# Kernel tuning notes

Measured on AMD Instinct MI355X. Metric: run time of the kernel, lower is better.

## Reference

```python
import jax, jax.numpy as jnp
import numpy as np

IGNORE_INDEX = 0


def _lovasz_softmax(inputs, targets):
    # inputs: [B, C, H, W] logits; targets: [B, H, W] int class ids
    C = inputs.shape[1]
    probs = jax.nn.softmax(inputs, axis=1)                      # [B,C,H,W]
    probs_flat = probs.transpose(0, 2, 3, 1).reshape(-1, C)     # [P,C]
    t = targets.reshape(-1)                                     # [P]
    valid = (t != IGNORE_INDEX)                                 # [P] bool

    # Per-class foreground indicator, zeroed at invalid pixels: [C,P]
    fg = ((t[None, :] == jnp.arange(C)[:, None]) & valid[None, :]).astype(probs_flat.dtype)
    # Errors |fg - prob|; invalid pixels forced to error 0 so they sort to the
    # end and contribute nothing (equivalent to filtering them out, since both
    # their error and the causal cumsums at earlier positions are unaffected).
    errors = jnp.abs(fg - probs_flat.T) * valid[None, :].astype(probs_flat.dtype)  # [C,P]

    # Sort each class's errors descending; permutation is non-differentiable (constant).
    order = jnp.argsort(-errors, axis=1)                        # [C,P]
    errors_sorted = jnp.take_along_axis(errors, order, axis=1)
    fg_sorted = jnp.take_along_axis(fg, order, axis=1)

    # Lovasz gradient (Alg. 1), vectorized over classes.
    gts = fg_sorted.sum(axis=1, keepdims=True)                  # [C,1]
    intersection = gts - jnp.cumsum(fg_sorted, axis=1)
    union = gts + jnp.cumsum(1.0 - fg_sorted, axis=1)
    jaccard = 1.0 - intersection / union                        # [C,P]
    grad = jnp.concatenate([jaccard[:, :1], jaccard[:, 1:] - jaccard[:, :-1]], axis=1)

    per_class = jnp.sum(jax.nn.relu(errors_sorted) * jax.lax.stop_gradient(grad), axis=1)  # [C]

    # classes='present': only classes with foreground among valid pixels, skip ignore_index.
    present = (fg.sum(axis=1) > 0) & (jnp.arange(C) != IGNORE_INDEX)  # [C] bool
    n_present = jnp.sum(present.astype(per_class.dtype))
    total = jnp.sum(jnp.where(present, per_class, 0.0))
    return jnp.where(n_present > 0, total / jnp.maximum(n_present, 1.0), 0.0)


def setup_inputs() -> dict:
    key = jax.random.key(0)
    k1, k2 = jax.random.split(key)
    B, C, H, W = 8, 8, 512, 512
    inputs = jax.random.normal(k1, (B, C, H, W), dtype=jnp.float32)
    targets = jax.random.randint(k2, (B, H, W), 0, C, dtype=jnp.int32)
    return {"inputs": inputs, "targets": targets}


def reference(inputs, targets):
    return _lovasz_softmax(inputs, targets)
```

## Files before the change

### kernel.cpp

```cpp
#include <hip/hip_runtime.h>
#include <stdint.h>

#define HW      262144
#define NCLASS  8
#define PIX     2097152
#define NCLS    7
#define KB      512
#define BLOCK   512
#define CHUNK   4096
#define NBLK    (PIX / CHUNK)
#define HSZ     (NCLS * KB)

__global__ __launch_bounds__(BLOCK) void lovasz_hist_kernel(
    const float* __restrict__ logits, const int* __restrict__ targets,
    unsigned long long* __restrict__ gNF)
{
    __shared__ unsigned int sPacked[HSZ];

    const int tid = threadIdx.x;
    for (int i = tid; i < HSZ; i += BLOCK) sPacked[i] = 0u;
    __syncthreads();

    const int base_p = blockIdx.x * CHUNK;
    #pragma unroll 1
    for (int it = 0; it < CHUNK / (BLOCK * 4); ++it) {
        const int p0 = base_p + it * (BLOCK * 4) + tid * 4;
        const int b  = p0 >> 18;
        const int hw = p0 & (HW - 1);
        const float* xp = logits + (size_t)b * (NCLASS * HW) + hw;

        const int4 t4 = *(const int4*)(targets + p0);
        float4 x4[NCLASS];
        #pragma unroll
        for (int c = 0; c < NCLASS; ++c)
            x4[c] = *(const float4*)(xp + (size_t)c * HW);

        const int tarr[4] = {t4.x, t4.y, t4.z, t4.w};
        #pragma unroll
        for (int j = 0; j < 4; ++j) {
            const int t = tarr[j];
            if (t == 0) continue;
            float x[NCLASS];
            #pragma unroll
            for (int c = 0; c < NCLASS; ++c)
                x[c] = (j == 0) ? x4[c].x : (j == 1) ? x4[c].y
                     : (j == 2) ? x4[c].z : x4[c].w;

            float m = x[0];
            #pragma unroll
            for (int c = 1; c < NCLASS; ++c) m = fmaxf(m, x[c]);
            float s = 0.0f;
            float ex[NCLASS];
            #pragma unroll
            for (int c = 0; c < NCLASS; ++c) { ex[c] = __expf(x[c] - m); s += ex[c]; }
            const float inv = 1.0f / s;
            #pragma unroll
            for (int c = 1; c < NCLASS; ++c) {
                const float pc = ex[c] * inv;
                const bool  fg = (t == c);
                const float err = fg ? (1.0f - pc) : pc;
                int k = (int)(err * (float)KB);
                k = (k > KB - 1) ? (KB - 1) : k;
                atomicAdd(&sPacked[(c - 1) * KB + k], fg ? 0x10001u : 1u);
            }
        }
    }
    __syncthreads();

    for (int i = tid; i < HSZ; i += BLOCK) {
        const unsigned pk = sPacked[i];
        if (pk) {
            const unsigned long long v =
                ((unsigned long long)(pk >> 16) << 32) | (unsigned long long)(pk & 0xFFFFu);
            atomicAdd(&gNF[i], v);
        }
    }
}

__global__ __launch_bounds__(NCLS * 64) void lovasz_scan_kernel(
    const unsigned long long* __restrict__ gNF, float* __restrict__ out)
{
    const int wid  = threadIdx.x >> 6;
    const int lane = threadIdx.x & 63;
    const unsigned long long* NF = gNF + wid * KB;

    unsigned int n[8], f[8];
    unsigned long long tnf = 0ull;
    #pragma unroll
    for (int j = 0; j < 8; ++j) {
        const int k = KB - 1 - (lane * 8 + j);
        const unsigned long long v = NF[k];
        n[j] = (unsigned)(v & 0xFFFFFFFFull);
        f[j] = (unsigned)(v >> 32);
        tnf += (unsigned long long)n[j] | ((unsigned long long)f[j] << 32);
    }

    unsigned long long inc = tnf;
    #pragma unroll
    for (int off = 1; off < 64; off <<= 1) {
        const unsigned long long u = __shfl_up(inc, off, 64);
        if (lane >= off) inc += u;
    }
    const unsigned long long tot = __shfl(inc, 63, 64);
    const unsigned int G = (unsigned)(tot >> 32);

    double contrib = 0.0;
    if (G > 0) {
        const unsigned long long exc = inc - tnf;
        long long i0 = (long long)(unsigned)(exc & 0xFFFFFFFFull);
        long long F0 = (long long)(unsigned)(exc >> 32);
        const long long Gl = (long long)G;
        #pragma unroll
        for (int j = 0; j < 8; ++j) {
            if (n[j]) {
                const long long i1 = i0 + n[j];
                const long long F1 = F0 + f[j];
                const long long num = (Gl - F0) * (Gl + i1 - F1)
                                    - (Gl - F1) * (Gl + i0 - F0);
                const double den = (double)(Gl + i0 - F0) * (double)(Gl + i1 - F1);
                const double dJ = (double)num / den;
                const double e = ((double)(KB - 1 - (lane * 8 + j)) + 0.5) / (double)KB;
                contrib += e * dJ;
            }
            i0 += n[j]; F0 += f[j];
        }
    }

    #pragma unroll
    for (int off = 32; off > 0; off >>= 1)
        contrib += __shfl_down(contrib, off, 64);

    __shared__ double sSum[NCLS];
    __shared__ int    sCnt[NCLS];
    if (lane == 0) { sSum[wid] = contrib; sCnt[wid] = (G > 0) ? 1 : 0; }
    __syncthreads();
    if (threadIdx.x == 0) {
        double s = 0.0; int cnt = 0;
        #pragma unroll
        for (int c = 0; c < NCLS; ++c) { s += sSum[c]; cnt += sCnt[c]; }
        out[0] = (cnt > 0) ? (float)(s / (double)cnt) : 0.0f;
    }
}

extern "C" void kernel_launch(void* const* d_in, const int* in_sizes, int n_in,
                              void* d_out, int out_size, void* d_ws, size_t ws_size,
                              hipStream_t stream) {
    const float* logits  = (const float*)d_in[0];
    const int*   targets = (const int*)d_in[1];
    float* out = (float*)d_out;
    unsigned long long* gNF = (unsigned long long*)d_ws;

    hipMemsetAsync(d_ws, 0, HSZ * sizeof(unsigned long long), stream);
    lovasz_hist_kernel<<<NBLK, BLOCK, 0, stream>>>(logits, targets, gNF);
    lovasz_scan_kernel<<<1, NCLS * 64, 0, stream>>>(gNF, out);
}
```

Measured before the change: 110.6 us.

## Fuse histogram and scan kernels via last-block completion counter

Merges the histogram and scan kernels into one launch: each block increments a global done counter and the last block to finish runs the per-class scan and final reduction, reading the histogram through atomics. Each thread now handles 8 pixels with all loads issued up front instead of two loop iterations of 4, and launch bounds request 4 blocks per CU. This removes one kernel launch and exposes more memory-level parallelism, at the cost of higher register pressure and a serialized tail in the last block.

After: 125.9 us. +13.9%, slower.

```diff
diff --git a/kernel.cpp b/kernel.cpp
--- a/kernel.cpp
+++ b/kernel.cpp
@@ -11,9 +11,13 @@
 #define NBLK    (PIX / CHUNK)
 #define HSZ     (NCLS * KB)
 
-__global__ __launch_bounds__(BLOCK) void lovasz_hist_kernel(
+#define OFF_DONE   28672
+#define ZERO_BYTES 28680
+
+__global__ __launch_bounds__(BLOCK, 4) void lovasz_fused_kernel(
     const float* __restrict__ logits, const int* __restrict__ targets,
-    unsigned long long* __restrict__ gNF)
+    unsigned long long* __restrict__ gNF, unsigned int* __restrict__ done,
+    float* __restrict__ out)
 {
     __shared__ unsigned int sPacked[HSZ];
 
@@ -21,48 +25,49 @@
     for (int i = tid; i < HSZ; i += BLOCK) sPacked[i] = 0u;
     __syncthreads();
 
-    const int base_p = blockIdx.x * CHUNK;
-    #pragma unroll 1
-    for (int it = 0; it < CHUNK / (BLOCK * 4); ++it) {
-        const int p0 = base_p + it * (BLOCK * 4) + tid * 4;
-        const int b  = p0 >> 18;
-        const int hw = p0 & (HW - 1);
-        const float* xp = logits + (size_t)b * (NCLASS * HW) + hw;
+    const int p0 = blockIdx.x * CHUNK + tid * 8;
+    const int b  = p0 >> 18;
+    const int hw = p0 & (HW - 1);
+    const float* xp = logits + (size_t)b * (NCLASS * HW) + hw;
 
-        const int4 t4 = *(const int4*)(targets + p0);
-        float4 x4[NCLASS];
+    const int4 tA = *(const int4*)(targets + p0);
+    const int4 tB = *(const int4*)(targets + p0 + 4);
+    float4 xa[NCLASS], xb[NCLASS];
+    #pragma unroll
+    for (int c = 0; c < NCLASS; ++c) {
+        xa[c] = *(const float4*)(xp + (size_t)c * HW);
+        xb[c] = *(const float4*)(xp + (size_t)c * HW + 4);
+    }
+
+    const int tarr[8] = {tA.x, tA.y, tA.z, tA.w, tB.x, tB.y, tB.z, tB.w};
+    #pragma unroll
+    for (int j = 0; j < 8; ++j) {
+        const int t = tarr[j];
+        if (t == 0) continue;
+        float x[NCLASS];
         #pragma unroll
-        for (int c = 0; c < NCLASS; ++c)
-            x4[c] = *(const float4*)(xp + (size_t)c * HW);
+        for (int c = 0; c < NCLASS; ++c) {
+            const float4 v = (j < 4) ? xa[c] : xb[c];
+            const int jj = j & 3;
+            x[c] = (jj == 0) ? v.x : (jj == 1) ? v.y : (jj == 2) ? v.z : v.w;
+        }
 
-        const int tarr[4] = {t4.x, t4.y, t4.z, t4.w};
+        float m = x[0];
         #pragma unroll
-        for (int j = 0; j < 4; ++j) {
-            const int t = tarr[j];
-            if (t == 0) continue;
-            float x[NCLASS];
-            #pragma unroll
-            for (int c = 0; c < NCLASS; ++c)
-                x[c] = (j == 0) ? x4[c].x : (j == 1) ? x4[c].y
-                     : (j == 2) ? x4[c].z : x4[c].w;
-
-            float m = x[0];
-            #pragma unroll
-            for (int c = 1; c < NCLASS; ++c) m = fmaxf(m, x[c]);
-            float s = 0.0f;
-            float ex[NCLASS];
-            #pragma unroll
-            for (int c = 0; c < NCLASS; ++c) { ex[c] = __expf(x[c] - m); s += ex[c]; }
-            const float inv = 1.0f / s;
-            #pragma unroll
-            for (int c = 1; c < NCLASS; ++c) {
-                const float pc = ex[c] * inv;
-                const bool  fg = (t == c);
-                const float err = fg ? (1.0f - pc) : pc;
-                int k = (int)(err * (float)KB);
-                k = (k > KB - 1) ? (KB - 1) : k;
-                atomicAdd(&sPacked[(c - 1) * KB + k], fg ? 0x10001u : 1u);
-            }
+        for (int c = 1; c < NCLASS; ++c) m = fmaxf(m, x[c]);
+        float s = 0.0f;
+        float ex[NCLASS];
+        #pragma unroll
+        for (int c = 0; c < NCLASS; ++c) { ex[c] = __expf(x[c] - m); s += ex[c]; }
+        const float inv = 1.0f / s;
+        #pragma unroll
+        for (int c = 1; c < NCLASS; ++c) {
+            const float pc = ex[c] * inv;
+            const bool  fg = (t == c);
+            const float err = fg ? (1.0f - pc) : pc;
+            int k = (int)(err * (float)KB);
+            k = (k > KB - 1) ? (KB - 1) : k;
+            atomicAdd(&sPacked[(c - 1) * KB + k], fg ? 0x10001u : 1u);
         }
     }
     __syncthreads();
@@ -75,66 +80,76 @@
             atomicAdd(&gNF[i], v);
         }
     }
-}
+    __syncthreads();
 
-__global__ __launch_bounds__(NCLS * 64) void lovasz_scan_kernel(
-    const unsigned long long* __restrict__ gNF, float* __restrict__ out)
-{
-    const int wid  = threadIdx.x >> 6;
-    const int lane = threadIdx.x & 63;
-    const unsigned long long* NF = gNF + wid * KB;
+    __shared__ unsigned int sLast;
+    if (tid == 0) {
+        __threadfence();
+        sLast = (atomicAdd(done, 1u) == NBLK - 1) ? 1u : 0u;
+    }
+    __syncthreads();
+    if (!sLast) return;
 
-    unsigned int n[8], f[8];
-    unsigned long long tnf = 0ull;
-    #pragma unroll
-    for (int j = 0; j < 8; ++j) {
-        const int k = KB - 1 - (lane * 8 + j);
-        const unsigned long long v = NF[k];
-        n[j] = (unsigned)(v & 0xFFFFFFFFull);
-        f[j] = (unsigned)(v >> 32);
-        tnf += (unsigned long long)n[j] | ((unsigned long long)f[j] << 32);
-    }
-
-    unsigned long long inc = tnf;
-    #pragma unroll
-    for (int off = 1; off < 64; off <<= 1) {
-        const unsigned long long u = __shfl_up(inc, off, 64);
-        if (lane >= off) inc += u;
-    }
-    const unsigned long long tot = __shfl(inc, 63, 64);
-    const unsigned int G = (unsigned)(tot >> 32);
-
-    double contrib = 0.0;
-    if (G > 0) {
-        const unsigned long long exc = inc - tnf;
-        long long i0 = (long long)(unsigned)(exc & 0xFFFFFFFFull);
-        long long F0 = (long long)(unsigned)(exc >> 32);
-        const long long Gl = (long long)G;
-        #pragma unroll
-        for (int j = 0; j < 8; ++j) {
-            if (n[j]) {
-                const long long i1 = i0 + n[j];
-                const long long F1 = F0 + f[j];
-                const long long num = (Gl - F0) * (Gl + i1 - F1)
-                                    - (Gl - F1) * (Gl + i0 - F0);
-                const double den = (double)(Gl + i0 - F0) * (double)(Gl + i1 - F1);
-                const double dJ = (double)num / den;
-                const double e = ((double)(KB - 1 - (lane * 8 + j)) + 0.5) / (double)KB;
-                contrib += e * dJ;
-            }
-            i0 += n[j]; F0 += f[j];
-        }
-    }
-
-    #pragma unroll
-    for (int off = 32; off > 0; off >>= 1)
-        contrib += __shfl_down(contrib, off, 64);
+    __threadfence();
+    const int wid  = tid >> 6;
+    const int lane = tid & 63;
 
     __shared__ double sSum[NCLS];
     __shared__ int    sCnt[NCLS];
-    if (lane == 0) { sSum[wid] = contrib; sCnt[wid] = (G > 0) ? 1 : 0; }
+
+    if (wid < NCLS) {
+        unsigned long long* NF = gNF + wid * KB;
+
+        unsigned int n[8], f[8];
+        unsigned long long tnf = 0ull;
+        #pragma unroll
+        for (int j = 0; j < 8; ++j) {
+            const int k = KB - 1 - (lane * 8 + j);
+            const unsigned long long v = atomicAdd(&NF[k], 0ull);
+            n[j] = (unsigned)(v & 0xFFFFFFFFull);
+            f[j] = (unsigned)(v >> 32);
+            tnf += (unsigned long long)n[j] | ((unsigned long long)f[j] << 32);
+        }
+
+        unsigned long long inc = tnf;
+        #pragma unroll
+        for (int off = 1; off < 64; off <<= 1) {
+            const unsigned long long u = __shfl_up(inc, off, 64);
+            if (lane >= off) inc += u;
+        }
+        const unsigned long long tot = __shfl(inc, 63, 64);
+        const unsigned int G = (unsigned)(tot >> 32);
+
+        double contrib = 0.0;
+        if (G > 0) {
+            const unsigned long long exc = inc - tnf;
+            long long i0 = (long long)(unsigned)(exc & 0xFFFFFFFFull);
+            long long F0 = (long long)(unsigned)(exc >> 32);
+            const long long Gl = (long long)G;
+            #pragma unroll
+            for (int j = 0; j < 8; ++j) {
+                if (n[j]) {
+                    const long long i1 = i0 + n[j];
+                    const long long F1 = F0 + f[j];
+                    const long long num = (Gl - F0) * (Gl + i1 - F1)
+                                        - (Gl - F1) * (Gl + i0 - F0);
+                    const double den = (double)(Gl + i0 - F0) * (double)(Gl + i1 - F1);
+                    const double dJ = (double)num / den;
+                    const double e = ((double)(KB - 1 - (lane * 8 + j)) + 0.5) / (double)KB;
+                    contrib += e * dJ;
+                }
+                i0 += n[j]; F0 += f[j];
+            }
+        }
+
+        #pragma unroll
+        for (int off = 32; off > 0; off >>= 1)
+            contrib += __shfl_down(contrib, off, 64);
+
+        if (lane == 0) { sSum[wid] = contrib; sCnt[wid] = (G > 0) ? 1 : 0; }
+    }
     __syncthreads();
-    if (threadIdx.x == 0) {
+    if (tid == 0) {
         double s = 0.0; int cnt = 0;
         #pragma unroll
         for (int c = 0; c < NCLS; ++c) { s += sSum[c]; cnt += sCnt[c]; }
@@ -148,9 +163,11 @@
     const float* logits  = (const float*)d_in[0];
     const int*   targets = (const int*)d_in[1];
     float* out = (float*)d_out;
-    unsigned long long* gNF = (unsigned long long*)d_ws;
 
-    hipMemsetAsync(d_ws, 0, HSZ * sizeof(unsigned long long), stream);
-    lovasz_hist_kernel<<<NBLK, BLOCK, 0, stream>>>(logits, targets, gNF);
-    lovasz_scan_kernel<<<1, NCLS * 64, 0, stream>>>(gNF, out);
+    uint8_t* ws = (uint8_t*)d_ws;
+    unsigned long long* gNF = (unsigned long long*)ws;
+    unsigned int* done      = (unsigned int*)(ws + OFF_DONE);
+
+    hipMemsetAsync(d_ws, 0, ZERO_BYTES, stream);
+    lovasz_fused_kernel<<<NBLK, BLOCK, 0, stream>>>(logits, targets, gNF, done, out);
 }
```
